# Kernel tuning notes

Hardware: AMD Instinct MI355X
Metric: run time of the kernel (lower is better)

Reference implementation:

```python
import jax, jax.numpy as jnp
import numpy as np

EPS = 1e-4
HEADS = 8
DIM_HEAD = 32
BALANCE = 0.3


def _normalize(x, dims):
    # torch normalize(): norm over `dims` in fp32; norm = eps + norm*sqrt(norm.numel()/x.numel())
    red = 1
    for d in dims:
        red *= x.shape[d]
    norm = jnp.sqrt(jnp.sum(jnp.square(x.astype(jnp.float32)), axis=dims, keepdims=True))
    norm = EPS + norm / np.sqrt(red)
    return x / norm.astype(x.dtype)


def _mpconv1x1(x, w, gain=1.0):
    # MPConv forward (eval mode): weight-normalize per output channel, scale, 1x1 conv
    w = w.astype(jnp.float32)
    w = _normalize(w, (1, 2, 3))
    fan_in = w.shape[1] * w.shape[2] * w.shape[3]
    w = (w * (gain / np.sqrt(fan_in))).astype(x.dtype)[:, :, 0, 0]  # [out, in]
    return jnp.einsum('oi,nihw->nohw', w, x)


def setup_inputs() -> dict:
    key = jax.random.key(0)
    k1, k2, k3 = jax.random.split(key, 3)
    x = jax.random.normal(k1, (2, 256, 48, 48), dtype=jnp.float32)
    w_qkv = jax.random.normal(k2, (768, 256, 1, 1), dtype=jnp.float32)
    w_out = jax.random.normal(k3, (256, 256, 1, 1), dtype=jnp.float32)
    return {"x": x, "w_qkv": w_qkv, "w_out": w_out}


def reference(x, w_qkv, w_out):
    n, c, h, w_sp = x.shape
    seq = h * w_sp
    y = _mpconv1x1(x, w_qkv)                          # [n, 3c, h, w]
    y = y.reshape(n, HEADS, DIM_HEAD, 3, seq)         # channel split: head x dim_head x 3
    y = _normalize(y, (2,))                           # L2-normalize over dim_head axis
    q = y[:, :, :, 0, :]
    k = y[:, :, :, 1, :]
    v = y[:, :, :, 2, :]
    # scores [n, h, q, k] with k scaled by 1/sqrt(dim_head)
    att = jax.nn.softmax(jnp.einsum('nhcq,nhck->nhqk', q, k) / np.sqrt(DIM_HEAD), axis=3)
    y = jnp.einsum('nhqk,nhck->nhcq', att, v)         # [n, heads, dim_head, seq]
    y = _mpconv1x1(y.reshape(n, c, h, w_sp), w_out)
    t = BALANCE
    # mp_sum: lerp then magnitude-preserving rescale
    return (x + t * (y - x)) / np.sqrt((1 - t) ** 2 + t ** 2)
```

## Files before the change

### kernel.cpp

```cpp
#include <hip/hip_runtime.h>
#include <math.h>

#define EPSN 1e-4f
#define SEQ 2304

using bf16x8 = __attribute__((ext_vector_type(8))) short;
using f32x4  = __attribute__((ext_vector_type(4))) float;

__device__ inline unsigned short f2bf(float x) {
    union { float f; unsigned u; } c; c.f = x;
    unsigned u = c.u;
    u += 0x7fffu + ((u >> 16) & 1u);
    return (unsigned short)(u >> 16);
}

__device__ inline unsigned cvt_pk_bf16(float lo, float hi) {
    unsigned r;
    asm("v_cvt_pk_bf16_f32 %0, %1, %2" : "=v"(r) : "v"(lo), "v"(hi));
    return r;
}

__global__ __launch_bounds__(256) void prep_kernel(const float* __restrict__ w_qkv,
                                                   const float* __restrict__ w_out,
                                                   const float* __restrict__ x,
                                                   unsigned short* __restrict__ wqb,
                                                   unsigned short* __restrict__ wob,
                                                   unsigned short* __restrict__ xt) {
    __shared__ __align__(16) unsigned short T[64][80];
    int bid = blockIdx.x;
    if (bid < 256) {
        int wave = threadIdx.x >> 6, lane = threadIdx.x & 63;
        int row = bid * 4 + wave;
        const float* src;
        unsigned short* dst;
        if (row < 768) { src = w_qkv + (size_t)row * 256; dst = wqb + (size_t)row * 256; }
        else           { src = w_out + (size_t)(row - 768) * 256; dst = wob + (size_t)(row - 768) * 256; }
        float4 v = *(const float4*)&src[lane * 4];
        float ss = v.x * v.x + v.y * v.y + v.z * v.z + v.w * v.w;
        for (int off = 32; off > 0; off >>= 1) ss += __shfl_xor(ss, off, 64);
        float sc = 1.0f / (sqrtf(ss) + 16.0f * EPSN);
        unsigned p0 = (unsigned)f2bf(v.x * sc) | ((unsigned)f2bf(v.y * sc) << 16);
        unsigned p1 = (unsigned)f2bf(v.z * sc) | ((unsigned)f2bf(v.w * sc) << 16);
        *(uint2*)&dst[lane * 4] = make_uint2(p0, p1);
    } else {
        int e0 = bid - 256;
        int st = e0 % 36, ct = (e0 / 36) & 3, n = e0 / 144;
        int t = threadIdx.x;
#pragma unroll
        for (int p = 0; p < 4; ++p) {
            int e = t + p * 256;
            int c = e >> 4, sv = (e & 15) * 4;
            float4 v = *(const float4*)&x[(size_t)(n * 256 + ct * 64 + c) * SEQ + st * 64 + sv];
            T[sv + 0][c] = f2bf(v.x);
            T[sv + 1][c] = f2bf(v.y);
            T[sv + 2][c] = f2bf(v.z);
            T[sv + 3][c] = f2bf(v.w);
        }
        __syncthreads();
#pragma unroll
        for (int p = 0; p < 2; ++p) {
            int e = t + p * 256;
            int s = e >> 3, cb = (e & 7) * 8;
            uint4 v = *(const uint4*)&T[s][cb];
            *(uint4*)&xt[(size_t)(n * SEQ + st * 64 + s) * 256 + ct * 64 + cb] = v;
        }
    }
}

__global__ __launch_bounds__(256) void qkv_fused_kernel(const unsigned short* __restrict__ xt,
                                                        const unsigned short* __restrict__ wqb,
                                                        unsigned short* __restrict__ qn,
                                                        unsigned short* __restrict__ kn,
                                                        unsigned short* __restrict__ vn) {
    __shared__ float Cs[96][65];
    int h  = blockIdx.x;
    int st = blockIdx.y;
    int n  = blockIdx.z;
    int tid = threadIdx.x;
    int wave = tid >> 6, lane = tid & 63;
    int ln = lane & 15, quad = lane >> 4;
    const unsigned short* Abase = wqb + (size_t)(h * 96 + ln) * 256 + quad * 8;
    const unsigned short* Bbase = xt + (size_t)(n * SEQ + st * 64 + wave * 16 + ln) * 256 + quad * 8;
    f32x4 acc[6];
#pragma unroll
    for (int m = 0; m < 6; ++m) acc[m] = (f32x4){0.f, 0.f, 0.f, 0.f};
#pragma unroll
    for (int kc = 0; kc < 8; ++kc) {
        bf16x8 b = *(const bf16x8*)(Bbase + kc * 32);
#pragma unroll
        for (int m = 0; m < 6; ++m) {
            bf16x8 a = *(const bf16x8*)(Abase + (size_t)(m * 16) * 256 + kc * 32);
            acc[m] = __builtin_amdgcn_mfma_f32_16x16x32_bf16(a, b, acc[m], 0, 0, 0);
        }
    }
#pragma unroll
    for (int m = 0; m < 6; ++m)
#pragma unroll
        for (int r = 0; r < 4; ++r)
            Cs[m * 16 + quad * 4 + r][wave * 16 + ln] = acc[m][r];
    __syncthreads();
    if (tid < 192) {
        int sl = tid & 63, wh = tid >> 6;
        int s = st * 64 + sl;
        int nh = n * 8 + h;
        float v[32];
        float ss = 0.f;
#pragma unroll
        for (int d = 0; d < 32; ++d) { v[d] = Cs[3 * d + wh][sl]; ss += v[d] * v[d]; }
        float inv = 1.0f / (EPSN + sqrtf(ss * (1.0f / 32.0f)));
        if (wh == 0) inv *= 0.17677669529663687f * 1.4426950408889634f;
        if (wh == 2) {
            unsigned short* dst = vn + (size_t)nh * 73728 + s;
#pragma unroll
            for (int d = 0; d < 32; ++d) dst[(size_t)d * SEQ] = f2bf(v[d] * inv);
        } else {
            unsigned short* dst = (wh == 1 ? kn : qn) + (size_t)nh * 73728 + (size_t)s * 32;
            unsigned wbuf[16];
#pragma unroll
            for (int j = 0; j < 16; ++j)
                wbuf[j] = (unsigned)f2bf(v[2 * j] * inv) | ((unsigned)f2bf(v[2 * j + 1] * inv) << 16);
#pragma unroll
            for (int j = 0; j < 4; ++j) {
                uint4 t4 = make_uint4(wbuf[4 * j], wbuf[4 * j + 1], wbuf[4 * j + 2], wbuf[4 * j + 3]);
                *(uint4*)(dst + j * 8) = t4;
            }
        }
    }
}

__global__ __launch_bounds__(256) void attn_mfma_kernel(const unsigned short* __restrict__ qn,
                                                        const unsigned short* __restrict__ kn,
                                                        const unsigned short* __restrict__ vn,
                                                        unsigned short* __restrict__ y2t) {
    __shared__ __align__(16) unsigned short Ks[2][64][40];
    __shared__ __align__(16) unsigned short Vs[2][32][72];
    __shared__ __align__(16) unsigned short Ps[4][16][72];
    __shared__ float Os[64][33];
    int tid = threadIdx.x;
    int wave = tid >> 6, lane = tid & 63;
    int ln = lane & 15, quad = lane >> 4;
    int qt = blockIdx.x, nh = blockIdx.y;
    int n = nh >> 3, h = nh & 7;
    const unsigned short* Qg = qn + (size_t)nh * 73728;
    const unsigned short* Kg = kn + (size_t)nh * 73728;
    const unsigned short* Vg = vn + (size_t)nh * 73728;

    bf16x8 qf = *(const bf16x8*)(Qg + (size_t)(qt * 64 + wave * 16 + ln) * 32 + quad * 8);
    bf16x8 ones;
#pragma unroll
    for (int i = 0; i < 8; ++i) ones[i] = (short)0x3F80;

    f32x4 o0 = {0.f, 0.f, 0.f, 0.f};
    f32x4 o1 = {0.f, 0.f, 0.f, 0.f};
    f32x4 lac = {0.f, 0.f, 0.f, 0.f};

    uint4 kreg = *(const uint4*)(Kg + (size_t)0 + tid * 8);
    uint4 vreg = *(const uint4*)(Vg + (size_t)(tid >> 3) * SEQ + (tid & 7) * 8);
    *(uint4*)(&Ks[0][tid >> 2][(tid & 3) * 8]) = kreg;
    *(uint4*)(&Vs[0][tid >> 3][(tid & 7) * 8]) = vreg;

    for (int i = 0; i < 36; ++i) {
        int buf = i & 1;
        if (i + 1 < 36) {
            int k0n = (i + 1) * 64;
            kreg = *(const uint4*)(Kg + (size_t)k0n * 32 + tid * 8);
            vreg = *(const uint4*)(Vg + (size_t)(tid >> 3) * SEQ + k0n + (tid & 7) * 8);
        }
        __syncthreads();

        const f32x4 zero = {0.f, 0.f, 0.f, 0.f};
#pragma unroll
        for (int c = 0; c < 4; ++c) {
            bf16x8 kf = *(const bf16x8*)(&Ks[buf][c * 16 + ln][quad * 8]);
            f32x4 sc = __builtin_amdgcn_mfma_f32_16x16x32_bf16(kf, qf, zero, 0, 0, 0);
            unsigned w0 = cvt_pk_bf16(exp2f(sc[0]), exp2f(sc[1]));
            unsigned w1 = cvt_pk_bf16(exp2f(sc[2]), exp2f(sc[3]));
            *(uint2*)(&Ps[wave][ln][c * 16 + quad * 4]) = make_uint2(w0, w1);
        }
#pragma unroll
        for (int kc = 0; kc < 2; ++kc) {
            bf16x8 pf = *(const bf16x8*)(&Ps[wave][ln][kc * 32 + quad * 8]);
            bf16x8 v0 = *(const bf16x8*)(&Vs[buf][ln][kc * 32 + quad * 8]);
            bf16x8 v1 = *(const bf16x8*)(&Vs[buf][16 + ln][kc * 32 + quad * 8]);
            lac = __builtin_amdgcn_mfma_f32_16x16x32_bf16(pf, ones, lac, 0, 0, 0);
            o0  = __builtin_amdgcn_mfma_f32_16x16x32_bf16(pf, v0, o0, 0, 0, 0);
            o1  = __builtin_amdgcn_mfma_f32_16x16x32_bf16(pf, v1, o1, 0, 0, 0);
        }
        if (i + 1 < 36) {
            *(uint4*)(&Ks[buf ^ 1][tid >> 2][(tid & 3) * 8]) = kreg;
            *(uint4*)(&Vs[buf ^ 1][tid >> 3][(tid & 7) * 8]) = vreg;
        }
    }

#pragma unroll
    for (int r = 0; r < 4; ++r) {
        int q = wave * 16 + quad * 4 + r;
        float inv = 1.0f / lac[r];
        Os[q][ln]      = o0[r] * inv;
        Os[q][16 + ln] = o1[r] * inv;
    }
    __syncthreads();
    {
        int q = tid >> 2, dg = tid & 3;
        const float* row = &Os[q][dg * 8];
        unsigned u0 = (unsigned)f2bf(row[0]) | ((unsigned)f2bf(row[1]) << 16);
        unsigned u1 = (unsigned)f2bf(row[2]) | ((unsigned)f2bf(row[3]) << 16);
        unsigned u2 = (unsigned)f2bf(row[4]) | ((unsigned)f2bf(row[5]) << 16);
        unsigned u3 = (unsigned)f2bf(row[6]) | ((unsigned)f2bf(row[7]) << 16);
        *(uint4*)&y2t[((size_t)(n * SEQ) + qt * 64 + q) * 256 + h * 32 + dg * 8] =
            make_uint4(u0, u1, u2, u3);
    }
}

__global__ __launch_bounds__(256) void out_gemm_kernel(const unsigned short* __restrict__ y2t,
                                                       const unsigned short* __restrict__ wob,
                                                       const float* __restrict__ x,
                                                       float* __restrict__ out) {
    int mt = blockIdx.x;
    int st = blockIdx.y;
    int n  = blockIdx.z;
    int tid = threadIdx.x;
    int wave = tid >> 6, lane = tid & 63;
    int ln = lane & 15, quad = lane >> 4;
    int m0 = mt * 64 + wave * 16;
    const unsigned short* Abase = wob + (size_t)(m0 + ln) * 256 + quad * 8;
    const unsigned short* Bbase = y2t + (size_t)(n * SEQ + st * 32 + ln) * 256 + quad * 8;
    f32x4 acc[2];
#pragma unroll
    for (int c = 0; c < 2; ++c) acc[c] = (f32x4){0.f, 0.f, 0.f, 0.f};
#pragma unroll
    for (int kc = 0; kc < 8; ++kc) {
        bf16x8 a = *(const bf16x8*)(Abase + kc * 32);
#pragma unroll
        for (int c = 0; c < 2; ++c) {
            bf16x8 b = *(const bf16x8*)(Bbase + (size_t)(c * 16) * 256 + kc * 32);
            acc[c] = __builtin_amdgcn_mfma_f32_16x16x32_bf16(a, b, acc[c], 0, 0, 0);
        }
    }
    const float c0f = 0.7f * 1.3130643285972254f;
    const float c1f = 0.3f * 1.3130643285972254f;
#pragma unroll
    for (int c = 0; c < 2; ++c)
#pragma unroll
        for (int r = 0; r < 4; ++r) {
            int o = m0 + quad * 4 + r;
            int s = st * 32 + c * 16 + ln;
            size_t idx = (size_t)(n * 256 + o) * SEQ + s;
            out[idx] = c0f * x[idx] + c1f * acc[c][r];
        }
}

extern "C" void kernel_launch(void* const* d_in, const int* in_sizes, int n_in,
                              void* d_out, int out_size, void* d_ws, size_t ws_size,
                              hipStream_t stream) {
    (void)in_sizes; (void)n_in; (void)out_size; (void)ws_size;
    const float* x     = (const float*)d_in[0];
    const float* w_qkv = (const float*)d_in[1];
    const float* w_out = (const float*)d_in[2];
    float* out = (float*)d_out;
    float* ws  = (float*)d_ws;
    unsigned short* wqb = (unsigned short*)(ws);
    unsigned short* wob = (unsigned short*)(ws + 98304);
    unsigned short* xt  = (unsigned short*)(ws + 131072);
    unsigned short* y2t = (unsigned short*)(ws + 131072);
    unsigned short* qn  = (unsigned short*)(ws + 720896);
    unsigned short* kn  = (unsigned short*)(ws + 1310720);
    unsigned short* vn  = (unsigned short*)(ws + 1900544);

    hipLaunchKernelGGL(prep_kernel, dim3(544), dim3(256), 0, stream,
                       w_qkv, w_out, x, wqb, wob, xt);
    hipLaunchKernelGGL(qkv_fused_kernel, dim3(8, 36, 2), dim3(256), 0, stream,
                       xt, wqb, qn, kn, vn);
    hipLaunchKernelGGL(attn_mfma_kernel, dim3(36, 16), dim3(256), 0, stream,
                       qn, kn, vn, y2t);
    hipLaunchKernelGGL(out_gemm_kernel, dim3(4, 72, 2), dim3(256), 0, stream,
                       y2t, wob, x, out);
}
```

Baseline: 138.0 us.

## Split attention keys across two wave groups, use permlane swaps, remap blocks per XCD

The attention kernel grows to 512 threads, and two groups of four waves each handle half of the key sequence. Their partial outputs and row sums are merged through shared memory at the end. The P matrix no longer round-trips through LDS: it is rearranged into MFMA operand layout in registers with permlane32/16 swaps. Block indices are remapped so that each XCD handles two heads, which should improve L2 reuse. The QKV kernel also stages V through LDS so its global stores are coalesced, at the cost of an extra barrier and more LDS per block.

```diff
diff --git a/kernel.cpp b/kernel.cpp
--- a/kernel.cpp
+++ b/kernel.cpp
@@ -18,6 +18,12 @@
     unsigned r;
     asm("v_cvt_pk_bf16_f32 %0, %1, %2" : "=v"(r) : "v"(lo), "v"(hi));
     return r;
+}
+__device__ inline void permlane32_swap(unsigned &a, unsigned &b) {
+    asm("v_permlane32_swap_b32 %0, %1" : "+v"(a), "+v"(b));
+}
+__device__ inline void permlane16_swap(unsigned &a, unsigned &b) {
+    asm("v_permlane16_swap_b32 %0, %1" : "+v"(a), "+v"(b));
 }
 
 __global__ __launch_bounds__(256) void prep_kernel(const float* __restrict__ w_qkv,
@@ -73,6 +79,7 @@
                                                         unsigned short* __restrict__ kn,
                                                         unsigned short* __restrict__ vn) {
     __shared__ float Cs[96][65];
+    __shared__ __align__(16) unsigned short Vls[32][72];
     int h  = blockIdx.x;
     int st = blockIdx.y;
     int n  = blockIdx.z;
@@ -99,10 +106,10 @@
         for (int r = 0; r < 4; ++r)
             Cs[m * 16 + quad * 4 + r][wave * 16 + ln] = acc[m][r];
     __syncthreads();
+    int nh = n * 8 + h;
     if (tid < 192) {
         int sl = tid & 63, wh = tid >> 6;
         int s = st * 64 + sl;
-        int nh = n * 8 + h;
         float v[32];
         float ss = 0.f;
 #pragma unroll
@@ -110,9 +117,8 @@
         float inv = 1.0f / (EPSN + sqrtf(ss * (1.0f / 32.0f)));
         if (wh == 0) inv *= 0.17677669529663687f * 1.4426950408889634f;
         if (wh == 2) {
-            unsigned short* dst = vn + (size_t)nh * 73728 + s;
-#pragma unroll
-            for (int d = 0; d < 32; ++d) dst[(size_t)d * SEQ] = f2bf(v[d] * inv);
+#pragma unroll
+            for (int d = 0; d < 32; ++d) Vls[d][sl] = f2bf(v[d] * inv);
         } else {
             unsigned short* dst = (wh == 1 ? kn : qn) + (size_t)nh * 73728 + (size_t)s * 32;
             unsigned wbuf[16];
@@ -126,26 +132,35 @@
             }
         }
     }
-}
-
-__global__ __launch_bounds__(256) void attn_mfma_kernel(const unsigned short* __restrict__ qn,
+    __syncthreads();
+    {
+        int d = tid >> 3, sj = (tid & 7) * 8;
+        uint4 t4 = *(const uint4*)&Vls[d][sj];
+        *(uint4*)&vn[(size_t)nh * 73728 + (size_t)d * SEQ + st * 64 + sj] = t4;
+    }
+}
+
+__global__ __launch_bounds__(512) void attn_mfma_kernel(const unsigned short* __restrict__ qn,
                                                         const unsigned short* __restrict__ kn,
                                                         const unsigned short* __restrict__ vn,
                                                         unsigned short* __restrict__ y2t) {
-    __shared__ __align__(16) unsigned short Ks[2][64][40];
-    __shared__ __align__(16) unsigned short Vs[2][32][72];
-    __shared__ __align__(16) unsigned short Ps[4][16][72];
-    __shared__ float Os[64][33];
+    __shared__ __align__(16) unsigned char SM[38912];
+    unsigned short (*Ks)[64][40] = (unsigned short (*)[64][40])SM;
+    unsigned short (*Vs)[32][72] = (unsigned short (*)[32][72])(SM + 20480);
     int tid = threadIdx.x;
     int wave = tid >> 6, lane = tid & 63;
     int ln = lane & 15, quad = lane >> 4;
-    int qt = blockIdx.x, nh = blockIdx.y;
+    int kg = wave >> 2, wq = wave & 3;
+    int bid = blockIdx.x;
+    int xcd = bid & 7, bi = bid >> 3;
+    int nh = xcd * 2 + (bi >= 36);
+    int qt = (bi >= 36) ? bi - 36 : bi;
     int n = nh >> 3, h = nh & 7;
     const unsigned short* Qg = qn + (size_t)nh * 73728;
     const unsigned short* Kg = kn + (size_t)nh * 73728;
     const unsigned short* Vg = vn + (size_t)nh * 73728;
 
-    bf16x8 qf = *(const bf16x8*)(Qg + (size_t)(qt * 64 + wave * 16 + ln) * 32 + quad * 8);
+    bf16x8 qf = *(const bf16x8*)(Qg + (size_t)(qt * 64 + wq * 16 + ln) * 32 + quad * 8);
     bf16x8 ones;
 #pragma unroll
     for (int i = 0; i < 8; ++i) ones[i] = (short)0x3F80;
@@ -154,61 +169,74 @@
     f32x4 o1 = {0.f, 0.f, 0.f, 0.f};
     f32x4 lac = {0.f, 0.f, 0.f, 0.f};
 
-    uint4 kreg = *(const uint4*)(Kg + (size_t)0 + tid * 8);
-    uint4 vreg = *(const uint4*)(Vg + (size_t)(tid >> 3) * SEQ + (tid & 7) * 8);
-    *(uint4*)(&Ks[0][tid >> 2][(tid & 3) * 8]) = kreg;
-    *(uint4*)(&Vs[0][tid >> 3][(tid & 7) * 8]) = vreg;
-
-    for (int i = 0; i < 36; ++i) {
+    int ts = tid & 255;
+    int kg2 = kg * 2;
+    int s0 = kg * 18 * 64;
+    uint4 kreg = *(const uint4*)(Kg + (size_t)s0 * 32 + ts * 8);
+    uint4 vreg = *(const uint4*)(Vg + (size_t)(ts >> 3) * SEQ + s0 + (ts & 7) * 8);
+    *(uint4*)(&Ks[kg2][ts >> 2][(ts & 3) * 8]) = kreg;
+    *(uint4*)(&Vs[kg2][ts >> 3][(ts & 7) * 8]) = vreg;
+
+    for (int i = 0; i < 18; ++i) {
         int buf = i & 1;
-        if (i + 1 < 36) {
-            int k0n = (i + 1) * 64;
-            kreg = *(const uint4*)(Kg + (size_t)k0n * 32 + tid * 8);
-            vreg = *(const uint4*)(Vg + (size_t)(tid >> 3) * SEQ + k0n + (tid & 7) * 8);
+        if (i + 1 < 18) {
+            int sn = s0 + (i + 1) * 64;
+            kreg = *(const uint4*)(Kg + (size_t)sn * 32 + ts * 8);
+            vreg = *(const uint4*)(Vg + (size_t)(ts >> 3) * SEQ + sn + (ts & 7) * 8);
         }
         __syncthreads();
 
         const f32x4 zero = {0.f, 0.f, 0.f, 0.f};
+        unsigned w[4][2];
 #pragma unroll
         for (int c = 0; c < 4; ++c) {
-            bf16x8 kf = *(const bf16x8*)(&Ks[buf][c * 16 + ln][quad * 8]);
+            bf16x8 kf = *(const bf16x8*)(&Ks[kg2 + buf][c * 16 + ln][quad * 8]);
             f32x4 sc = __builtin_amdgcn_mfma_f32_16x16x32_bf16(kf, qf, zero, 0, 0, 0);
-            unsigned w0 = cvt_pk_bf16(exp2f(sc[0]), exp2f(sc[1]));
-            unsigned w1 = cvt_pk_bf16(exp2f(sc[2]), exp2f(sc[3]));
-            *(uint2*)(&Ps[wave][ln][c * 16 + quad * 4]) = make_uint2(w0, w1);
+            w[c][0] = cvt_pk_bf16(exp2f(sc[0]), exp2f(sc[1]));
+            w[c][1] = cvt_pk_bf16(exp2f(sc[2]), exp2f(sc[3]));
         }
 #pragma unroll
         for (int kc = 0; kc < 2; ++kc) {
-            bf16x8 pf = *(const bf16x8*)(&Ps[wave][ln][kc * 32 + quad * 8]);
-            bf16x8 v0 = *(const bf16x8*)(&Vs[buf][ln][kc * 32 + quad * 8]);
-            bf16x8 v1 = *(const bf16x8*)(&Vs[buf][16 + ln][kc * 32 + quad * 8]);
-            lac = __builtin_amdgcn_mfma_f32_16x16x32_bf16(pf, ones, lac, 0, 0, 0);
-            o0  = __builtin_amdgcn_mfma_f32_16x16x32_bf16(pf, v0, o0, 0, 0, 0);
-            o1  = __builtin_amdgcn_mfma_f32_16x16x32_bf16(pf, v1, o1, 0, 0, 0);
-        }
-        if (i + 1 < 36) {
-            *(uint4*)(&Ks[buf ^ 1][tid >> 2][(tid & 3) * 8]) = kreg;
-            *(uint4*)(&Vs[buf ^ 1][tid >> 3][(tid & 7) * 8]) = vreg;
-        }
-    }
-
+            unsigned a0 = w[2 * kc][0], b0 = w[2 * kc + 1][0];
+            permlane32_swap(a0, b0);
+            permlane16_swap(a0, b0);
+            unsigned a1 = w[2 * kc][1], b1 = w[2 * kc + 1][1];
+            permlane32_swap(a1, b1);
+            permlane16_swap(a1, b1);
+            union { unsigned u[4]; bf16x8 v8; } pk;
+            pk.u[0] = a0; pk.u[1] = a1; pk.u[2] = b0; pk.u[3] = b1;
+            bf16x8 v0 = *(const bf16x8*)(&Vs[kg2 + buf][ln][kc * 32 + quad * 8]);
+            bf16x8 v1 = *(const bf16x8*)(&Vs[kg2 + buf][16 + ln][kc * 32 + quad * 8]);
+            lac = __builtin_amdgcn_mfma_f32_16x16x32_bf16(pk.v8, ones, lac, 0, 0, 0);
+            o0  = __builtin_amdgcn_mfma_f32_16x16x32_bf16(pk.v8, v0, o0, 0, 0, 0);
+            o1  = __builtin_amdgcn_mfma_f32_16x16x32_bf16(pk.v8, v1, o1, 0, 0, 0);
+        }
+        if (i + 1 < 18) {
+            *(uint4*)(&Ks[kg2 + (buf ^ 1)][ts >> 2][(ts & 3) * 8]) = kreg;
+            *(uint4*)(&Vs[kg2 + (buf ^ 1)][ts >> 3][(ts & 7) * 8]) = vreg;
+        }
+    }
+
+    __syncthreads();
+    float (*Os)[36] = (float (*)[36])SM;
+    float* Ls = (float*)(SM + 128 * 36 * 4);
 #pragma unroll
     for (int r = 0; r < 4; ++r) {
-        int q = wave * 16 + quad * 4 + r;
-        float inv = 1.0f / lac[r];
-        Os[q][ln]      = o0[r] * inv;
-        Os[q][16 + ln] = o1[r] * inv;
+        int q = wq * 16 + quad * 4 + r;
+        Os[kg * 64 + q][ln] = o0[r];
+        Os[kg * 64 + q][16 + ln] = o1[r];
+        if (ln == 0) Ls[kg * 64 + q] = lac[r];
     }
     __syncthreads();
     {
-        int q = tid >> 2, dg = tid & 3;
-        const float* row = &Os[q][dg * 8];
-        unsigned u0 = (unsigned)f2bf(row[0]) | ((unsigned)f2bf(row[1]) << 16);
-        unsigned u1 = (unsigned)f2bf(row[2]) | ((unsigned)f2bf(row[3]) << 16);
-        unsigned u2 = (unsigned)f2bf(row[4]) | ((unsigned)f2bf(row[5]) << 16);
-        unsigned u3 = (unsigned)f2bf(row[6]) | ((unsigned)f2bf(row[7]) << 16);
-        *(uint4*)&y2t[((size_t)(n * SEQ) + qt * 64 + q) * 256 + h * 32 + dg * 8] =
-            make_uint4(u0, u1, u2, u3);
+        int q = tid >> 3, dg = (tid & 7) * 4;
+        float inv = 1.0f / (Ls[q] + Ls[64 + q]);
+        float r0 = (Os[q][dg + 0] + Os[64 + q][dg + 0]) * inv;
+        float r1 = (Os[q][dg + 1] + Os[64 + q][dg + 1]) * inv;
+        float r2 = (Os[q][dg + 2] + Os[64 + q][dg + 2]) * inv;
+        float r3 = (Os[q][dg + 3] + Os[64 + q][dg + 3]) * inv;
+        *(uint2*)&y2t[((size_t)(n * SEQ) + qt * 64 + q) * 256 + h * 32 + dg] =
+            make_uint2(cvt_pk_bf16(r0, r1), cvt_pk_bf16(r2, r3));
     }
 }
 
@@ -271,7 +299,7 @@
                        w_qkv, w_out, x, wqb, wob, xt);
     hipLaunchKernelGGL(qkv_fused_kernel, dim3(8, 36, 2), dim3(256), 0, stream,
                        xt, wqb, qn, kn, vn);
-    hipLaunchKernelGGL(attn_mfma_kernel, dim3(36, 16), dim3(256), 0, stream,
+    hipLaunchKernelGGL(attn_mfma_kernel, dim3(576), dim3(512), 0, stream,
                        qn, kn, vn, y2t);
     hipLaunchKernelGGL(out_gemm_kernel, dim3(4, 72, 2), dim3(256), 0, stream,
                        y2t, wob, x, out);
```

Result: faster. 133.7 us (-3.1%).
